# Kernel tuning notes

Measured on AMD Instinct MI355X. Metric: run time of the kernel, lower is better.

The kernel has to match this reference:

```python
import jax, jax.numpy as jnp
import numpy as np

N_HEAD = 6


def setup_inputs() -> dict:
    key = jax.random.key(0)
    k1, k2, k3 = jax.random.split(key, 3)
    B, N, D = 16, 512, 768
    d_head = D // N_HEAD
    p_mask = jnp.ones((B, N), dtype=jnp.float32)
    feature = jax.random.normal(k1, (B, N, D), dtype=jnp.float32)
    # nn.Linear weights (out, in); scaled like torch default init
    W = jax.random.normal(k2, (D, D), dtype=jnp.float32) / np.sqrt(D)
    # attn Linear(2*d_head -> n_head); only the diagonal head rows are used
    Wa = jax.random.normal(k3, (N_HEAD, 2 * d_head), dtype=jnp.float32) / np.sqrt(2 * d_head)
    return {"p_mask": p_mask, "feature": feature, "W": W, "Wa": Wa, "num_layers": 2}


def reference(p_mask, feature, W, Wa, num_layers):
    B, N, D = feature.shape
    H = N_HEAD
    Dh = D // H
    # adj[b,q,k] = p_mask[b,q] * p_mask[b,k]  (bmm of unsqueezed mask)
    adj = p_mask[:, :, None] * p_mask[:, None, :]  # (B,N,N)
    mask = adj[:, :, :, None] > 0                   # (B,N,N,1)
    for _ in range(num_layers):
        residual = feature
        qk = (feature @ W.T).reshape(B, N, H, Dh)  # (B,N,H,Dh)
        # concat(q,k) @ Wa[h] decomposes into query part + key part
        sq = jnp.einsum('bqhd,hd->bqh', qk, Wa[:, :Dh])
        sk = jnp.einsum('bkhd,hd->bkh', qk, Wa[:, Dh:])
        score = jnp.tanh(sq[:, :, None, :] + sk[:, None, :, :])  # (B,N,N,H)
        # masked_fill with -1e-8 where adj == 0 (faithful to source)
        score = jnp.where(mask, score, jnp.float32(-1e-8))
        attn = jax.nn.softmax(score, axis=2)  # softmax over key dim (dim=-2)
        # dropout p=0 in eval -> identity
        hid = jnp.tanh(jnp.einsum('bqkh,bkhd->bqhd', attn, qk))  # (B,N,H,Dh)
        feature = residual + hid.reshape(B, N, D)
    return feature
```

## Files before the change

### kernel.cpp

```cpp
#include <hip/hip_runtime.h>
#include <hip/hip_bf16.h>
#include <stdint.h>

#define BATCH 16
#define NSEQ  512
#define DMODEL 768
#define NHEAD 6
#define DHEAD 128
#define MROWS (BATCH * NSEQ)
#define QBLK  32
#define KTILE 64

typedef __attribute__((ext_vector_type(8))) __bf16 bf16x8;
typedef __attribute__((ext_vector_type(4))) __bf16 bf16x4;
typedef __attribute__((ext_vector_type(4))) float  f32x4;
typedef __attribute__((ext_vector_type(4))) unsigned int u32x4;

#define GLD16(gp, lp) __builtin_amdgcn_global_load_lds( \
    (const __attribute__((address_space(1))) unsigned int*)(gp), \
    (__attribute__((address_space(3))) unsigned int*)(lp), 16, 0, 0)

#define BAR_PLAIN() do { asm volatile("" ::: "memory"); \
    __builtin_amdgcn_s_barrier(); asm volatile("" ::: "memory"); } while (0)
#define BAR_LGKM() do { asm volatile("s_waitcnt lgkmcnt(0)" ::: "memory"); \
    __builtin_amdgcn_s_barrier(); asm volatile("" ::: "memory"); } while (0)

__global__ void cvt_bf16_kernel(const float* __restrict__ src,
                                __bf16* __restrict__ dst, int n4) {
    int i = blockIdx.x * blockDim.x + threadIdx.x;
    if (i < n4) {
        float4 v = reinterpret_cast<const float4*>(src)[i];
        bf16x4 o;
        o.x = (__bf16)v.x; o.y = (__bf16)v.y; o.z = (__bf16)v.z; o.w = (__bf16)v.w;
        reinterpret_cast<bf16x4*>(dst)[i] = o;
    }
}

template<bool AFP32>
__global__ __launch_bounds__(256) void gemm_bt(const void* __restrict__ Av,
                                               const __bf16* __restrict__ Bm,
                                               __bf16* __restrict__ C,
                                               const float* __restrict__ Wa,
                                               const float* __restrict__ pmask,
                                               float* __restrict__ eq_t,
                                               float* __restrict__ ek_t) {
    const __bf16* Ab = reinterpret_cast<const __bf16*>(Av);
    const float*  Af = reinterpret_cast<const float*>(Av);

    __shared__ __align__(16) __bf16 As[2][AFP32 ? 4096 : 2048];
    __shared__ __align__(16) __bf16 Bs[2][128 * 32];
    const int tid  = threadIdx.x;
    const int lane = tid & 63;
    const int wave = tid >> 6;
    const int wm = wave >> 1, wn = wave & 1;

    const int wg  = blockIdx.x;
    const int nid = (wg & 7) * 96 + (wg >> 3);
    const int bx  = nid % 6;
    const int by  = nid / 6;
    const int m0 = by * 64;
    const int n0 = bx * 128;

    f32x4 acc[2][4] = {};

    const int e0   = tid * 8;
    const int row0 = tid >> 2;
    const int k0i  = (tid & 3) * 8;

    const int lr = lane & 15;
    const int lg = lane >> 4;
    const int kb = lg * 8;

    auto STAGE = [&](int kt, int bufi) {
        if constexpr (AFP32) {
            #pragma unroll
            for (int i2 = 0; i2 < 2; i2++) {
                int tt  = tid + 256 * i2;
                int row = tt >> 3;
                int k0s = ((tt & 7) * 4) ^ ((row & 7) << 2);
                GLD16(Af + (size_t)(m0 + row) * DMODEL + kt + k0s,
                      reinterpret_cast<float*>(&As[bufi][0]) + tt * 4);
            }
        } else {
            GLD16(Ab + (size_t)(m0 + row0) * DMODEL + kt + k0i, &As[bufi][e0]);
        }
        GLD16(Bm + (size_t)(n0 + row0)      * DMODEL + kt + k0i, &Bs[bufi][e0]);
        GLD16(Bm + (size_t)(n0 + row0 + 64) * DMODEL + kt + k0i, &Bs[bufi][e0 + 2048]);
    };

    STAGE(0, 0);

    for (int t = 0; t < 24; t++) {
        const int buf = t & 1;
        if (t < 23) {
            STAGE((t + 1) * 32, buf ^ 1);
            if constexpr (AFP32) asm volatile("s_waitcnt vmcnt(4)" ::: "memory");
            else                 asm volatile("s_waitcnt vmcnt(3)" ::: "memory");
        } else {
            asm volatile("s_waitcnt vmcnt(0)" ::: "memory");
        }
        __builtin_amdgcn_s_barrier();
        asm volatile("" ::: "memory");

        bf16x8 af[2], bfv[4];
        if constexpr (AFP32) {
            const float* A32 = reinterpret_cast<const float*>(&As[buf][0]);
            const int sw = (lr & 7) << 2;
            #pragma unroll
            for (int i = 0; i < 2; i++) {
                int row = wm * 32 + i * 16 + lr;
                f32x4 lo = *reinterpret_cast<const f32x4*>(&A32[row * 32 + (kb ^ sw)]);
                f32x4 hi = *reinterpret_cast<const f32x4*>(&A32[row * 32 + ((kb + 4) ^ sw)]);
                #pragma unroll
                for (int j = 0; j < 4; j++) {
                    af[i][j]     = (__bf16)lo[j];
                    af[i][4 + j] = (__bf16)hi[j];
                }
            }
        } else {
            #pragma unroll
            for (int i = 0; i < 2; i++)
                af[i] = *reinterpret_cast<const bf16x8*>(&As[buf][(wm * 32 + i * 16 + lr) * 32 + kb]);
        }
        #pragma unroll
        for (int j = 0; j < 4; j++)
            bfv[j] = *reinterpret_cast<const bf16x8*>(&Bs[buf][(wn * 64 + j * 16 + lr) * 32 + kb]);
        #pragma unroll
        for (int i = 0; i < 2; i++)
            #pragma unroll
            for (int j = 0; j < 4; j++)
                acc[i][j] = __builtin_amdgcn_mfma_f32_16x16x32_bf16(af[i], bfv[j], acc[i][j], 0, 0, 0);

        BAR_PLAIN();
    }

    const int rg = lg * 4;
    #pragma unroll
    for (int i = 0; i < 2; i++) {
        #pragma unroll
        for (int j = 0; j < 4; j++) {
            #pragma unroll
            for (int r = 0; r < 4; r++) {
                int row = m0 + wm * 32 + i * 16 + rg + r;
                int col = n0 + wn * 64 + j * 16 + lr;
                C[(size_t)row * DMODEL + col] = (__bf16)acc[i][j][r];
            }
        }
    }

    const int h = bx;
    float wqv[4], wkv[4];
    #pragma unroll
    for (int j = 0; j < 4; j++) {
        int d = wn * 64 + j * 16 + lr;
        wqv[j] = Wa[h * 256 + d];
        wkv[j] = Wa[h * 256 + 128 + d];
    }
    float* red = reinterpret_cast<float*>(&As[0][0]);
    #pragma unroll
    for (int i = 0; i < 2; i++) {
        #pragma unroll
        for (int r = 0; r < 4; r++) {
            float aq = 0.f, ak = 0.f;
            #pragma unroll
            for (int j = 0; j < 4; j++) {
                aq += acc[i][j][r] * wqv[j];
                ak += acc[i][j][r] * wkv[j];
            }
            #pragma unroll
            for (int off = 1; off < 16; off <<= 1) {
                aq += __shfl_xor(aq, off);
                ak += __shfl_xor(ak, off);
            }
            if (lr == 0) {
                int row = wm * 32 + i * 16 + rg + r;
                red[(0 * 64 + row) * 2 + wn] = aq;
                red[(1 * 64 + row) * 2 + wn] = ak;
            }
        }
    }
    __syncthreads();
    if (tid < 64) {
        int row = m0 + tid;
        float s = red[tid * 2] + red[tid * 2 + 1];
        eq_t[(size_t)h * MROWS + row] = (pmask[row] > 0.f) ? __expf(2.f * s) : 0.f;
    } else if (tid < 128) {
        int rl  = tid - 64;
        int row = m0 + rl;
        float s = red[(64 + rl) * 2] + red[(64 + rl) * 2 + 1];
        ek_t[(size_t)h * MROWS + row] = (pmask[row] > 0.f) ? __expf(2.f * s) : 0.f;
    }
}

template<int LAYER>
__global__ __launch_bounds__(256) void attn_pv(const __bf16* __restrict__ QK,
                                               const float* __restrict__ eq_t,
                                               const float* __restrict__ ek_t,
                                               const float* __restrict__ resf,
                                               const __bf16* __restrict__ resb,
                                               float* __restrict__ outf,
                                               __bf16* __restrict__ outb) {
    const int wg  = blockIdx.x;
    const int nid = (wg & 7) * 192 + (wg >> 3);
    const int qt = nid & 15;
    const int hb = nid >> 4;
    const int h  = hb % NHEAD;
    const int b  = hb / NHEAD;
    const int q0 = qt * QBLK;

    __shared__ __align__(16) __bf16 w[QBLK][512];
    __shared__ __align__(16) __bf16 Vt[4][32 * KTILE];
    const int tid  = threadIdx.x;
    const int lane = tid & 63;
    const int wave = tid >> 6;

    const int wd0 = wave * 32;
    const int lr  = lane & 15;
    const int lg  = lane >> 4;

    const int kg = lane >> 2;
    const int dg = lane & 3;
    const __bf16* Vbase = QK + (size_t)b * NSEQ * DMODEL + (size_t)h * DHEAD + wd0 + dg * 8;
    char* vtw = reinterpret_cast<char*>(&Vt[0][0]) + wave * 4096;

    u32x4 A0, A1, A2, A3, B0, B1, B2, B3;
    #define LOADS(S0, S1, S2, S3, t) do { \
        const __bf16* p = Vbase + (size_t)((t) * KTILE + kg * 4) * DMODEL; \
        S0 = *reinterpret_cast<const u32x4*>(p); \
        S1 = *reinterpret_cast<const u32x4*>(p + DMODEL); \
        S2 = *reinterpret_cast<const u32x4*>(p + 2 * DMODEL); \
        S3 = *reinterpret_cast<const u32x4*>(p + 3 * DMODEL); \
    } while (0)
    #define WRITEV(S0, S1, S2, S3) do { \
        _Pragma("unroll") \
        for (int j = 0; j < 8; j++) { \
            int dl = dg * 8 + j; \
            int sw = j ^ dg; \
            unsigned sel = (j & 1) ? 0x07060302u : 0x05040100u; \
            unsigned lo = __builtin_amdgcn_perm(S1[j >> 1], S0[j >> 1], sel); \
            unsigned hi = __builtin_amdgcn_perm(S3[j >> 1], S2[j >> 1], sel); \
            unsigned long long pk = (unsigned long long)lo | ((unsigned long long)hi << 32); \
            *reinterpret_cast<unsigned long long*>(vtw + dl * 128 + (((kg * 4) ^ (sw << 3)) * 2)) = pk; \
        } \
    } while (0)

    LOADS(A0, A1, A2, A3, 0);
    LOADS(B0, B1, B2, B3, 1);

    float res[2][4][2];
    #pragma unroll
    for (int qh = 0; qh < 2; qh++) {
        #pragma unroll
        for (int r = 0; r < 4; r++) {
            int ql = qh * 16 + lg * 4 + r;
            #pragma unroll
            for (int n = 0; n < 2; n++) {
                int d = wd0 + n * 16 + lr;
                size_t o = ((size_t)(b * NSEQ + q0 + ql)) * DMODEL + (size_t)h * DHEAD + d;
                if constexpr (LAYER == 0) res[qh][r][n] = resf[o];
                else                      res[qh][r][n] = (float)resb[o];
            }
        }
    }

    const int k0 = lane * 8;
    const size_t sbase = (size_t)h * MROWS + b * NSEQ;
    float4 e0v = *reinterpret_cast<const float4*>(&ek_t[sbase + k0]);
    float4 e1v = *reinterpret_cast<const float4*>(&ek_t[sbase + k0 + 4]);
    float ek[8] = {e0v.x, e0v.y, e0v.z, e0v.w, e1v.x, e1v.y, e1v.z, e1v.w};
    float eq[8];
    #pragma unroll
    for (int g = 0; g < 8; g++)
        eq[g] = eq_t[sbase + q0 + wave * 8 + g];

    WRITEV(A0, A1, A2, A3);
    LOADS(A0, A1, A2, A3, 2);

    #pragma unroll
    for (int g = 0; g < 8; g++) {
        int q = wave * 8 + g;
        float eqv = eq[g];
        bf16x8 wv;
        #pragma unroll
        for (int j = 0; j < 8; j++) {
            float u = eqv * ek[j];
            float z = __builtin_amdgcn_rcpf(u + 1.f);
            float p = __expf(fmaf(z, -2.f, 1.f));
            wv[j] = (__bf16)(u > 0.f ? p : 1.0f);
        }
        *reinterpret_cast<bf16x8*>(&w[q][k0 ^ ((q & 7) << 3)]) = wv;
    }
    BAR_LGKM();

    bf16x8 vones;
    #pragma unroll
    for (int e = 0; e < 8; e++) vones[e] = (__bf16)1.0f;

    f32x4 acc[2][2] = {};
    f32x4 accs[2] = {};

    const int wswz = (lr & 7) << 3;

    #pragma unroll
    for (int t = 0; t < 8; t++) {
        __builtin_amdgcn_s_setprio(1);
        #pragma unroll
        for (int ks = 0; ks < 2; ks++) {
            int cb = (t * 64 + ks * 32 + lg * 8) ^ wswz;
            bf16x8 af0 = *reinterpret_cast<const bf16x8*>(&w[lr][cb]);
            bf16x8 af1 = *reinterpret_cast<const bf16x8*>(&w[16 + lr][cb]);
            #pragma unroll
            for (int n = 0; n < 2; n++) {
                int dl   = n * 16 + lr;
                int sw   = (dl & 7) ^ ((dl >> 3) & 7);
                bf16x8 bv = *reinterpret_cast<const bf16x8*>(
                    vtw + dl * 128 + (((ks * 4 + lg) ^ sw) << 4));
                acc[0][n] = __builtin_amdgcn_mfma_f32_16x16x32_bf16(af0, bv, acc[0][n], 0, 0, 0);
                acc[1][n] = __builtin_amdgcn_mfma_f32_16x16x32_bf16(af1, bv, acc[1][n], 0, 0, 0);
            }
            accs[0] = __builtin_amdgcn_mfma_f32_16x16x32_bf16(af0, vones, accs[0], 0, 0, 0);
            accs[1] = __builtin_amdgcn_mfma_f32_16x16x32_bf16(af1, vones, accs[1], 0, 0, 0);
        }
        __builtin_amdgcn_s_setprio(0);
        if (t < 7) {
            __builtin_amdgcn_sched_barrier(0);
            asm volatile("s_waitcnt lgkmcnt(0)" ::: "memory");
            if ((t & 1) == 0) WRITEV(B0, B1, B2, B3);
            else              WRITEV(A0, A1, A2, A3);
        }
        if (t < 5) {
            if ((t & 1) == 0) LOADS(B0, B1, B2, B3, t + 3);
            else              LOADS(A0, A1, A2, A3, t + 3);
        }
    }

    #pragma unroll
    for (int qh = 0; qh < 2; qh++) {
        #pragma unroll
        for (int r = 0; r < 4; r++) {
            int ql = qh * 16 + lg * 4 + r;
            float rden = __builtin_amdgcn_rcpf(accs[qh][r]);
            #pragma unroll
            for (int n = 0; n < 2; n++) {
                int d  = wd0 + n * 16 + lr;
                float hv = acc[qh][n][r] * rden;
                float e2 = __expf(2.f * hv);
                float tv = 1.f - 2.f * __builtin_amdgcn_rcpf(e2 + 1.f);
                size_t o = ((size_t)(b * NSEQ + q0 + ql)) * DMODEL + (size_t)h * DHEAD + d;
                float ov = res[qh][r][n] + tv;
                if constexpr (LAYER == 0) outb[o] = (__bf16)ov;
                else                      outf[o] = ov;
            }
        }
    }
    #undef LOADS
    #undef WRITEV
}

extern "C" void kernel_launch(void* const* d_in, const int* in_sizes, int n_in,
                              void* d_out, int out_size, void* d_ws, size_t ws_size,
                              hipStream_t stream) {
    const float* pmask   = (const float*)d_in[0];
    const float* feature = (const float*)d_in[1];
    const float* W       = (const float*)d_in[2];
    const float* Wa      = (const float*)d_in[3];
    float* out = (float*)d_out;
    char* ws = (char*)d_ws;

    __bf16* Abf  = (__bf16*)ws;
    __bf16* Wbf  = (__bf16*)(ws + 12582912);
    __bf16* QKbf = (__bf16*)(ws + 12582912 + 1179648);
    float*  eq   = (float*)(ws + 12582912 + 1179648 + 12582912);
    float*  ek   = eq + MROWS * NHEAD;

    const int wN4 = (DMODEL * DMODEL) / 4;

    hipLaunchKernelGGL(cvt_bf16_kernel, dim3((wN4 + 255) / 256), dim3(256), 0, stream,
                       W, Wbf, wN4);

    hipLaunchKernelGGL((gemm_bt<true>), dim3(768), dim3(256), 0, stream,
                       (const void*)feature, Wbf, QKbf, Wa, pmask, eq, ek);
    hipLaunchKernelGGL((attn_pv<0>), dim3(1536), dim3(256), 0, stream,
                       QKbf, eq, ek, feature, (const __bf16*)nullptr,
                       (float*)nullptr, Abf);

    hipLaunchKernelGGL((gemm_bt<false>), dim3(768), dim3(256), 0, stream,
                       (const void*)Abf, Wbf, QKbf, Wa, pmask, eq, ek);
    hipLaunchKernelGGL((attn_pv<1>), dim3(1536), dim3(256), 0, stream,
                       QKbf, eq, ek, (const float*)nullptr, Abf,
                       out, (__bf16*)nullptr);
}
```

Before: 99.16 us.

## Compute softmax denominators via shuffles and restructure GEMM double-buffer barriers

```diff
diff --git a/kernel.cpp b/kernel.cpp
--- a/kernel.cpp
+++ b/kernel.cpp
@@ -20,9 +20,9 @@
     (const __attribute__((address_space(1))) unsigned int*)(gp), \
     (__attribute__((address_space(3))) unsigned int*)(lp), 16, 0, 0)
 
-#define BAR_PLAIN() do { asm volatile("" ::: "memory"); \
+#define BAR_LGKM() do { asm volatile("s_waitcnt lgkmcnt(0)" ::: "memory"); \
     __builtin_amdgcn_s_barrier(); asm volatile("" ::: "memory"); } while (0)
-#define BAR_LGKM() do { asm volatile("s_waitcnt lgkmcnt(0)" ::: "memory"); \
+#define BAR_VM0() do { asm volatile("s_waitcnt vmcnt(0)" ::: "memory"); \
     __builtin_amdgcn_s_barrier(); asm volatile("" ::: "memory"); } while (0)
 
 __global__ void cvt_bf16_kernel(const float* __restrict__ src,
@@ -89,18 +89,11 @@
     };
 
     STAGE(0, 0);
+    BAR_VM0();
 
     for (int t = 0; t < 24; t++) {
         const int buf = t & 1;
-        if (t < 23) {
-            STAGE((t + 1) * 32, buf ^ 1);
-            if constexpr (AFP32) asm volatile("s_waitcnt vmcnt(4)" ::: "memory");
-            else                 asm volatile("s_waitcnt vmcnt(3)" ::: "memory");
-        } else {
-            asm volatile("s_waitcnt vmcnt(0)" ::: "memory");
-        }
-        __builtin_amdgcn_s_barrier();
-        asm volatile("" ::: "memory");
+        if (t < 23) STAGE((t + 1) * 32, buf ^ 1);
 
         bf16x8 af[2], bfv[4];
         if constexpr (AFP32) {
@@ -131,7 +124,7 @@
             for (int j = 0; j < 4; j++)
                 acc[i][j] = __builtin_amdgcn_mfma_f32_16x16x32_bf16(af[i], bfv[j], acc[i][j], 0, 0, 0);
 
-        BAR_PLAIN();
+        BAR_VM0();
     }
 
     const int rg = lg * 4;
@@ -210,6 +203,7 @@
 
     __shared__ __align__(16) __bf16 w[QBLK][512];
     __shared__ __align__(16) __bf16 Vt[4][32 * KTILE];
+    __shared__ float rdenLds[QBLK];
     const int tid  = threadIdx.x;
     const int lane = tid & 63;
     const int wave = tid >> 6;
@@ -276,28 +270,39 @@
     WRITEV(A0, A1, A2, A3);
     LOADS(A0, A1, A2, A3, 2);
 
+    float psum[8];
     #pragma unroll
     for (int g = 0; g < 8; g++) {
         int q = wave * 8 + g;
         float eqv = eq[g];
         bf16x8 wv;
+        float ps = 0.f;
         #pragma unroll
         for (int j = 0; j < 8; j++) {
             float u = eqv * ek[j];
             float z = __builtin_amdgcn_rcpf(u + 1.f);
             float p = __expf(fmaf(z, -2.f, 1.f));
-            wv[j] = (__bf16)(u > 0.f ? p : 1.0f);
-        }
+            float wf = (u > 0.f ? p : 1.0f);
+            ps += wf;
+            wv[j] = (__bf16)wf;
+        }
+        psum[g] = ps;
         *reinterpret_cast<bf16x8*>(&w[q][k0 ^ ((q & 7) << 3)]) = wv;
     }
+    #pragma unroll
+    for (int off = 1; off < 64; off <<= 1) {
+        #pragma unroll
+        for (int g = 0; g < 8; g++)
+            psum[g] += __shfl_xor(psum[g], off);
+    }
+    if (lane == 0) {
+        #pragma unroll
+        for (int g = 0; g < 8; g++)
+            rdenLds[wave * 8 + g] = __builtin_amdgcn_rcpf(psum[g]);
+    }
     BAR_LGKM();
 
-    bf16x8 vones;
-    #pragma unroll
-    for (int e = 0; e < 8; e++) vones[e] = (__bf16)1.0f;
-
     f32x4 acc[2][2] = {};
-    f32x4 accs[2] = {};
 
     const int wswz = (lr & 7) << 3;
 
@@ -318,8 +323,6 @@
                 acc[0][n] = __builtin_amdgcn_mfma_f32_16x16x32_bf16(af0, bv, acc[0][n], 0, 0, 0);
                 acc[1][n] = __builtin_amdgcn_mfma_f32_16x16x32_bf16(af1, bv, acc[1][n], 0, 0, 0);
             }
-            accs[0] = __builtin_amdgcn_mfma_f32_16x16x32_bf16(af0, vones, accs[0], 0, 0, 0);
-            accs[1] = __builtin_amdgcn_mfma_f32_16x16x32_bf16(af1, vones, accs[1], 0, 0, 0);
         }
         __builtin_amdgcn_s_setprio(0);
         if (t < 7) {
@@ -339,7 +342,7 @@
         #pragma unroll
         for (int r = 0; r < 4; r++) {
             int ql = qh * 16 + lg * 4 + r;
-            float rden = __builtin_amdgcn_rcpf(accs[qh][r]);
+            float rden = rdenLds[ql];
             #pragma unroll
             for (int n = 0; n < 2; n++) {
                 int d  = wd0 + n * 16 + lr;
```

Result: slower. 103.2 us (+4.0%).
